# Optimization experiments

Hardware: AMD Instinct MI355X
Metric: run time of the kernel (lower is better)

Reference implementation:

```python
import jax, jax.numpy as jnp
import numpy as np

N_NODES = 100000
N_EDGES = 1600000
EDGES_IN = 1
HID = 64
OUT = 64


def setup_inputs() -> dict:
    key = jax.random.key(0)
    ks = jax.random.split(key, 10)
    s = lambda fan_in: 1.0 / np.sqrt(fan_in)
    inp = {
        "edge_index": jax.random.randint(ks[0], (2, N_EDGES), 0, N_NODES, dtype=jnp.int64) if jax.config.jax_enable_x64 else jax.random.randint(ks[0], (2, N_EDGES), 0, N_NODES, dtype=jnp.int32),
        "edge_attr": jax.random.normal(ks[1], (N_EDGES, EDGES_IN), dtype=jnp.float32),
        # edge MLP: Linear(EDGES_IN->HID), SiLU, Linear(HID->HID), SiLU
        "W1": jax.random.uniform(ks[2], (EDGES_IN, HID), jnp.float32, -s(EDGES_IN), s(EDGES_IN)),
        "b1": jax.random.uniform(ks[3], (HID,), jnp.float32, -s(EDGES_IN), s(EDGES_IN)),
        "W2": jax.random.uniform(ks[4], (HID, HID), jnp.float32, -s(HID), s(HID)),
        "b2": jax.random.uniform(ks[5], (HID,), jnp.float32, -s(HID), s(HID)),
        # node MLP: Linear(HID->HID), SiLU, Linear(HID->OUT)
        "W3": jax.random.uniform(ks[6], (HID, HID), jnp.float32, -s(HID), s(HID)),
        "b3": jax.random.uniform(ks[7], (HID,), jnp.float32, -s(HID), s(HID)),
        "W4": jax.random.uniform(ks[8], (HID, OUT), jnp.float32, -s(HID), s(HID)),
        "b4": jax.random.uniform(ks[9], (OUT,), jnp.float32, -s(HID), s(HID)),
    }
    return inp


def reference(edge_index, edge_attr, W1, b1, W2, b2, W3, b3, W4, b4):
    silu = jax.nn.silu
    # edge model: [E, EDGES_IN] -> [E, HID]
    ef = silu(edge_attr @ W1 + b1)
    ef = silu(ef @ W2 + b2)
    # unsorted_segment_sum over source nodes (row): [E, HID] -> [N, HID]
    row = edge_index[0]
    agg = jax.ops.segment_sum(ef, row, num_segments=N_NODES)
    # node model: [N, HID] -> [N, OUT]
    h = silu(agg @ W3 + b3) @ W4 + b4
    return h
```

## Files before the change

kernel.cpp:

```cpp
#include <hip/hip_runtime.h>
#include <math.h>
#include <utility>

#define TN 4096
#define XMIN (-8.0f)
#define XMAX (8.0f)

#define GB1 256
#define MAXBK 2048
#define BKN 64
#define BKCAP 1792

typedef __attribute__((ext_vector_type(8))) short short8;
typedef __attribute__((ext_vector_type(4))) float f32x4;

__device__ __forceinline__ float silu_f(float v) {
    return v / (1.0f + __expf(-v));
}

__device__ __forceinline__ unsigned short f2bf(float x) {
    unsigned u = __float_as_uint(x);
    return (unsigned short)((u + 0x7FFFu + ((u >> 16) & 1u)) >> 16);
}
__device__ __forceinline__ float bf2f(unsigned short h) {
    return __uint_as_float(((unsigned)h) << 16);
}

#define SPLIT8(w0,w1,w2,w3,w4,w5,w6,w7, H, L) { \
    unsigned short _h0=f2bf(w0),_h1=f2bf(w1),_h2=f2bf(w2),_h3=f2bf(w3), \
                   _h4=f2bf(w4),_h5=f2bf(w5),_h6=f2bf(w6),_h7=f2bf(w7); \
    H = (short8){(short)_h0,(short)_h1,(short)_h2,(short)_h3, \
                 (short)_h4,(short)_h5,(short)_h6,(short)_h7}; \
    L = (short8){(short)f2bf((w0)-bf2f(_h0)),(short)f2bf((w1)-bf2f(_h1)), \
                 (short)f2bf((w2)-bf2f(_h2)),(short)f2bf((w3)-bf2f(_h3)), \
                 (short)f2bf((w4)-bf2f(_h4)),(short)f2bf((w5)-bf2f(_h5)), \
                 (short)f2bf((w6)-bf2f(_h6)),(short)f2bf((w7)-bf2f(_h7))}; }

#define BFRAG(Wp, kc, nt, H, L) { \
    const float* _p = (Wp) + ((kc)*32 + quad*8)*64 + (nt)*16 + m; \
    SPLIT8(_p[0],_p[64],_p[128],_p[192],_p[256],_p[320],_p[384],_p[448], H, L) }

#define MFMA3(AH, AL, BH, BL, ACC) \
    ACC = __builtin_amdgcn_mfma_f32_16x16x32_bf16(AH, BH, ACC, 0, 0, 0); \
    ACC = __builtin_amdgcn_mfma_f32_16x16x32_bf16(AL, BH, ACC, 0, 0, 0); \
    ACC = __builtin_amdgcn_mfma_f32_16x16x32_bf16(AH, BL, ACC, 0, 0, 0);

__global__ void build_table_k(const float* __restrict__ W1, const float* __restrict__ b1,
                              const float* __restrict__ W2, const float* __restrict__ b2,
                              float* __restrict__ table2, int* __restrict__ cnt, int nbk) {
    int gid  = blockIdx.x * blockDim.x + threadIdx.x;
    if (gid < nbk) cnt[gid] = 0;
    int wave = gid >> 6;
    int lane = gid & 63;
    if (wave >= TN) return;
    const float step = (XMAX - XMIN) / (float)(TN - 1);
    float x  = XMIN + step * (float)wave;
    float h1 = silu_f(fmaf(x, W1[lane], b1[lane]));
    float acc = b2[lane];
#pragma unroll
    for (int k = 0; k < 64; ++k) {
        float h1k = __shfl(h1, k, 64);
        acc = fmaf(h1k, W2[k * 64 + lane], acc);
    }
    float val = silu_f(acc);
    table2[(size_t)wave * 128 + 2 * lane] = val;
    if (wave > 0)
        table2[(size_t)(wave - 1) * 128 + 2 * lane + 1] = val;
}

__global__ void pack_w_k(const float* __restrict__ W3, const float* __restrict__ W4,
                         short8* __restrict__ packW) {
    int t = threadIdx.x, lane = t & 63, wid = t >> 6;
    int m = lane & 15, quad = lane >> 4;
    for (int f = wid; f < 16; f += 4) {
        const float* Wp = (f < 8) ? W3 : W4;
        int kc = f & 1, nt = (f >> 1) & 3;
        short8 H, L;
        BFRAG(Wp, kc, nt, H, L)
        packW[(2 * f + 0) * 64 + lane] = H;
        packW[(2 * f + 1) * 64 + lane] = L;
    }
}

__global__ void bhist_k(const int* __restrict__ row, int* __restrict__ cnt,
                        int E, int nbk) {
    __shared__ int h[MAXBK];
    int t = threadIdx.x;
    for (int e = t; e < nbk; e += 256) h[e] = 0;
    __syncthreads();
    for (int i = blockIdx.x * 256 + t; i < E; i += 256 * GB1)
        atomicAdd(&h[row[i] >> 6], 1);
    __syncthreads();
    for (int e = t; e < nbk; e += 256)
        if (h[e]) atomicAdd(&cnt[e], h[e]);
}

__global__ void scan1_k(const int* __restrict__ cnt, int* __restrict__ bhs,
                        int* __restrict__ cur, int n) {
    __shared__ int b0[MAXBK], b1[MAXBK];
    int t = threadIdx.x;
    for (int e = t; e < MAXBK; e += 1024) b0[e] = (e < n) ? cnt[e] : 0;
    __syncthreads();
    int* src = b0; int* dst = b1;
    for (int d = 1; d < MAXBK; d <<= 1) {
        for (int e = t; e < MAXBK; e += 1024)
            dst[e] = src[e] + ((e >= d) ? src[e - d] : 0);
        __syncthreads();
        int* tmp = src; src = dst; dst = tmp;
    }
    for (int e = t; e < n; e += 1024) {
        int v = (e == 0) ? 0 : src[e - 1];
        bhs[e] = v; cur[e] = v;
    }
    if (t == 0) bhs[n] = src[n - 1];
}

__global__ void bscatter_k(const int* __restrict__ row, const float* __restrict__ x,
                           int* __restrict__ cur, unsigned int* __restrict__ packed,
                           int E, int nbk) {
    __shared__ int hist[MAXBK];
    int t = threadIdx.x;
    for (int e = t; e < nbk; e += 256) hist[e] = 0;
    __syncthreads();
    for (int i = blockIdx.x * 256 + t; i < E; i += 256 * GB1)
        atomicAdd(&hist[row[i] >> 6], 1);
    __syncthreads();
    int shift = (int)(((long)blockIdx.x * nbk) >> 8);
    for (int k = t; k < nbk; k += 256) {
        int e = k + shift; if (e >= nbk) e -= nbk;
        int c = hist[e];
        hist[e] = c ? atomicAdd(&cur[e], c) : 0;
    }
    __syncthreads();
    const float scale = (float)(TN - 1) / (XMAX - XMIN);
    for (int i = blockIdx.x * 256 + t; i < E; i += 256 * GB1) {
        int   r  = row[i];
        float xv = x[i];
        float tt = fminf(fmaxf((xv - XMIN) * scale, 0.f), (float)(TN - 1) - 0.001f);
        int   i0 = (int)tt;
        unsigned int q = min((unsigned int)((tt - (float)i0) * 8192.0f), 8191u);
        unsigned int pk = ((unsigned int)(r & 63) << 25) | ((unsigned int)i0 << 13) | q;
        int p = atomicAdd(&hist[r >> 6], 1);
        packed[p] = pk;
    }
}

__global__ __launch_bounds__(256, 8)
void gather_k(const unsigned int* __restrict__ packed, const int* __restrict__ bhs,
              const float* __restrict__ table2, float* __restrict__ aggOut, int N) {
    __shared__ __align__(16) unsigned int srt[BKCAP];
    __shared__ int hist[BKN + 1];
    __shared__ int curs[BKN];
    int t = threadIdx.x, lane = t & 63, wid = t >> 6;
    int b = blockIdx.x;

    int s   = bhs[b];
    int e_  = bhs[b + 1];
    int cnt = min(e_ - s, BKCAP);

    for (int i = t; i <= BKN; i += 256) hist[i] = 0;
    __syncthreads();
    for (int i = t; i < cnt; i += 256)
        atomicAdd(&hist[packed[s + i] >> 25], 1);
    __syncthreads();

    if (wid == 0) {
        int c = hist[lane];
        int sc = c;
#pragma unroll
        for (int d = 1; d < 64; d <<= 1) {
            int u = __shfl_up(sc, d, 64);
            if (lane >= d) sc += u;
        }
        hist[lane] = sc - c;  curs[lane] = sc - c;
        if (lane == 63) hist[BKN] = sc;
    }
    __syncthreads();

    for (int i = t; i < cnt; i += 256) {
        unsigned int p = packed[s + i];
        int pos = atomicAdd(&curs[p >> 25], 1);
        srt[pos] = p;
    }
    __syncthreads();

    const float2* tab = (const float2*)table2 + lane;
    for (int nl = wid; nl < BKN; nl += 4) {
        int n = (b << 6) + nl;
        if (n >= N) break;
        int beg = hist[nl], dn = hist[nl + 1] - beg;
        float a0 = 0.f, a1 = 0.f, a2 = 0.f, a3 = 0.f;
        int j = 0;
        int head = (4 - (beg & 3)) & 3;
        if (head > dn) head = dn;
        for (; j < head; ++j) {
            unsigned int p0 = srt[beg + j];
            float2 uv0 = tab[(size_t)((p0 >> 13) & 0xFFFu) << 6];
            float f0 = (float)(p0 & 0x1FFFu) * (1.0f / 8192.0f);
            a0 = fmaf(f0, uv0.y - uv0.x, a0 + uv0.x);
        }
        for (; j + 4 <= dn; j += 4) {
            uint4 q = *(const uint4*)&srt[beg + j];
            unsigned int p0 = q.x, p1 = q.y, p2 = q.z, p3 = q.w;
            float2 uv0 = tab[(size_t)((p0 >> 13) & 0xFFFu) << 6];
            float2 uv1 = tab[(size_t)((p1 >> 13) & 0xFFFu) << 6];
            float2 uv2 = tab[(size_t)((p2 >> 13) & 0xFFFu) << 6];
            float2 uv3 = tab[(size_t)((p3 >> 13) & 0xFFFu) << 6];
            float f0 = (float)(p0 & 0x1FFFu) * (1.0f / 8192.0f);
            float f1 = (float)(p1 & 0x1FFFu) * (1.0f / 8192.0f);
            float f2 = (float)(p2 & 0x1FFFu) * (1.0f / 8192.0f);
            float f3 = (float)(p3 & 0x1FFFu) * (1.0f / 8192.0f);
            a0 = fmaf(f0, uv0.y - uv0.x, a0 + uv0.x);
            a1 = fmaf(f1, uv1.y - uv1.x, a1 + uv1.x);
            a2 = fmaf(f2, uv2.y - uv2.x, a2 + uv2.x);
            a3 = fmaf(f3, uv3.y - uv3.x, a3 + uv3.x);
        }
        for (; j < dn; ++j) {
            unsigned int p0 = srt[beg + j];
            float2 uv0 = tab[(size_t)((p0 >> 13) & 0xFFFu) << 6];
            float f0 = (float)(p0 & 0x1FFFu) * (1.0f / 8192.0f);
            a0 = fmaf(f0, uv0.y - uv0.x, a0 + uv0.x);
        }
        aggOut[(size_t)n * 64 + lane] = (a0 + a1) + (a2 + a3);
    }
}

__global__ __launch_bounds__(256, 1)
void mlp_k(const short8* __restrict__ packW, const float* __restrict__ b3,
           const float* __restrict__ b4, float* __restrict__ h, int N, int ntiles) {
    __shared__ float gt[4][16 * 68];
    int t = threadIdx.x, lane = t & 63, wid = t >> 6;
    int m = lane & 15, quad = lane >> 4;

    const short8* pw = packW + lane;
#define LDW(s) pw[(s) * 64]
    short8 B3h00=LDW( 0), B3l00=LDW( 1), B3h01=LDW( 2), B3l01=LDW( 3);
    short8 B3h10=LDW( 4), B3l10=LDW( 5), B3h11=LDW( 6), B3l11=LDW( 7);
    short8 B3h20=LDW( 8), B3l20=LDW( 9), B3h21=LDW(10), B3l21=LDW(11);
    short8 B3h30=LDW(12), B3l30=LDW(13), B3h31=LDW(14), B3l31=LDW(15);
    short8 B4h00=LDW(16), B4l00=LDW(17), B4h01=LDW(18), B4l01=LDW(19);
    short8 B4h10=LDW(20), B4l10=LDW(21), B4h11=LDW(22), B4l11=LDW(23);
    short8 B4h20=LDW(24), B4l20=LDW(25), B4h21=LDW(26), B4l21=LDW(27);
    short8 B4h30=LDW(28), B4l30=LDW(29), B4h31=LDW(30), B4l31=LDW(31);
#undef LDW
    float c0 = b4[0*16 + m], c1 = b4[1*16 + m], c2 = b4[2*16 + m], c3 = b4[3*16 + m];
    float d0 = b3[0*16 + m], d1 = b3[1*16 + m], d2 = b3[2*16 + m], d3 = b3[3*16 + m];
    float* g = gt[wid];

    for (int tile = blockIdx.x; tile < ntiles; tile += gridDim.x) {
        long r0 = (long)tile * 64 + wid * 16;
        if (r0 >= N) continue;

        long ra = r0 + m; if (ra > N - 1) ra = N - 1;
        const float* ap = h + ra * 64 + quad * 8;
        float4 p0 = *(const float4*)(ap);       float4 p1 = *(const float4*)(ap + 4);
        float4 p2 = *(const float4*)(ap + 32);  float4 p3 = *(const float4*)(ap + 36);
        short8 Ah0, Al0, Ah1, Al1;
        SPLIT8(p0.x,p0.y,p0.z,p0.w,p1.x,p1.y,p1.z,p1.w, Ah0, Al0)
        SPLIT8(p2.x,p2.y,p2.z,p2.w,p3.x,p3.y,p3.z,p3.w, Ah1, Al1)

        f32x4 acc0 = {0.f,0.f,0.f,0.f}, acc1 = {0.f,0.f,0.f,0.f};
        f32x4 acc2 = {0.f,0.f,0.f,0.f}, acc3 = {0.f,0.f,0.f,0.f};
        MFMA3(Ah0, Al0, B3h00, B3l00, acc0)  MFMA3(Ah1, Al1, B3h01, B3l01, acc0)
        MFMA3(Ah0, Al0, B3h10, B3l10, acc1)  MFMA3(Ah1, Al1, B3h11, B3l11, acc1)
        MFMA3(Ah0, Al0, B3h20, B3l20, acc2)  MFMA3(Ah1, Al1, B3h21, B3l21, acc2)
        MFMA3(Ah0, Al0, B3h30, B3l30, acc3)  MFMA3(Ah1, Al1, B3h31, B3l31, acc3)

        g[(quad*4+0)*68 + 0*16 + m] = silu_f(acc0.x + d0);
        g[(quad*4+1)*68 + 0*16 + m] = silu_f(acc0.y + d0);
        g[(quad*4+2)*68 + 0*16 + m] = silu_f(acc0.z + d0);
        g[(quad*4+3)*68 + 0*16 + m] = silu_f(acc0.w + d0);
        g[(quad*4+0)*68 + 1*16 + m] = silu_f(acc1.x + d1);
        g[(quad*4+1)*68 + 1*16 + m] = silu_f(acc1.y + d1);
        g[(quad*4+2)*68 + 1*16 + m] = silu_f(acc1.z + d1);
        g[(quad*4+3)*68 + 1*16 + m] = silu_f(acc1.w + d1);
        g[(quad*4+0)*68 + 2*16 + m] = silu_f(acc2.x + d2);
        g[(quad*4+1)*68 + 2*16 + m] = silu_f(acc2.y + d2);
        g[(quad*4+2)*68 + 2*16 + m] = silu_f(acc2.z + d2);
        g[(quad*4+3)*68 + 2*16 + m] = silu_f(acc2.w + d2);
        g[(quad*4+0)*68 + 3*16 + m] = silu_f(acc3.x + d3);
        g[(quad*4+1)*68 + 3*16 + m] = silu_f(acc3.y + d3);
        g[(quad*4+2)*68 + 3*16 + m] = silu_f(acc3.z + d3);
        g[(quad*4+3)*68 + 3*16 + m] = silu_f(acc3.w + d3);

        const float* gp = g + m * 68 + quad * 8;
        float4 q0 = *(const float4*)(gp);       float4 q1 = *(const float4*)(gp + 4);
        float4 q2 = *(const float4*)(gp + 32);  float4 q3 = *(const float4*)(gp + 36);
        short8 Gh0, Gl0, Gh1, Gl1;
        SPLIT8(q0.x,q0.y,q0.z,q0.w,q1.x,q1.y,q1.z,q1.w, Gh0, Gl0)
        SPLIT8(q2.x,q2.y,q2.z,q2.w,q3.x,q3.y,q3.z,q3.w, Gh1, Gl1)

        f32x4 o0 = {0.f,0.f,0.f,0.f}, o1 = {0.f,0.f,0.f,0.f};
        f32x4 o2 = {0.f,0.f,0.f,0.f}, o3 = {0.f,0.f,0.f,0.f};
        MFMA3(Gh0, Gl0, B4h00, B4l00, o0)  MFMA3(Gh1, Gl1, B4h01, B4l01, o0)
        MFMA3(Gh0, Gl0, B4h10, B4l10, o1)  MFMA3(Gh1, Gl1, B4h11, B4l11, o1)
        MFMA3(Gh0, Gl0, B4h20, B4l20, o2)  MFMA3(Gh1, Gl1, B4h21, B4l21, o2)
        MFMA3(Gh0, Gl0, B4h30, B4l30, o3)  MFMA3(Gh1, Gl1, B4h31, B4l31, o3)

        long rw = r0 + quad * 4;
        if (rw + 0 < N) { float* o = h + (rw+0)*64;
            o[ 0+m]=o0.x+c0; o[16+m]=o1.x+c1; o[32+m]=o2.x+c2; o[48+m]=o3.x+c3; }
        if (rw + 1 < N) { float* o = h + (rw+1)*64;
            o[ 0+m]=o0.y+c0; o[16+m]=o1.y+c1; o[32+m]=o2.y+c2; o[48+m]=o3.y+c3; }
        if (rw + 2 < N) { float* o = h + (rw+2)*64;
            o[ 0+m]=o0.z+c0; o[16+m]=o1.z+c1; o[32+m]=o2.z+c2; o[48+m]=o3.z+c3; }
        if (rw + 3 < N) { float* o = h + (rw+3)*64;
            o[ 0+m]=o0.w+c0; o[16+m]=o1.w+c1; o[32+m]=o2.w+c2; o[48+m]=o3.w+c3; }
    }
}

__global__ void zero_k(float4* __restrict__ p, int n4) {
    int i = blockIdx.x * blockDim.x + threadIdx.x;
    int stride = gridDim.x * blockDim.x;
    float4 z = make_float4(0.f, 0.f, 0.f, 0.f);
    for (; i < n4; i += stride) p[i] = z;
}

__global__ void edge_k(const int* __restrict__ row, const float* __restrict__ xarr,
                       const float* __restrict__ table2, float* __restrict__ agg, int E) {
    int gid    = blockIdx.x * blockDim.x + threadIdx.x;
    int lane   = gid & 63;
    int wave   = gid >> 6;
    int nwaves = (gridDim.x * blockDim.x) >> 6;
    const float scale = (float)(TN - 1) / (XMAX - XMIN);
    const float2* tab = (const float2*)table2 + lane;
    for (int e = wave; e < E; e += nwaves) {
        float x = xarr[e];
        int   r = row[e];
        float t = fminf(fmaxf((x - XMIN) * scale, 0.0f), (float)(TN - 1) - 0.001f);
        int   i0 = (int)t;
        float f  = t - (float)i0;
        float2 uv = tab[i0 << 6];
        atomicAdd(agg + (size_t)r * 64 + lane, fmaf(f, uv.y - uv.x, uv.x));
    }
}

extern "C" void kernel_launch(void* const* d_in, const int* in_sizes, int n_in,
                              void* d_out, int out_size, void* d_ws, size_t ws_size,
                              hipStream_t stream) {
    const int*   edge_index = (const int*)  d_in[0];
    const float* edge_attr  = (const float*)d_in[1];
    const float* W1 = (const float*)d_in[2];
    const float* b1 = (const float*)d_in[3];
    const float* W2 = (const float*)d_in[4];
    const float* b2 = (const float*)d_in[5];
    const float* W3 = (const float*)d_in[6];
    const float* b3 = (const float*)d_in[7];
    const float* W4 = (const float*)d_in[8];
    const float* b4 = (const float*)d_in[9];

    float* out = (float*)d_out;
    const int E   = in_sizes[1];
    const int N   = out_size / 64;
    const int nbk = (N + 63) >> 6;
    const int nmb = (N + 63) / 64;

    char* ws = (char*)d_ws;
    size_t off = 0;
    auto carve = [&](size_t bytes) { size_t r = off; off = (off + bytes + 255) & ~(size_t)255; return r; };
    size_t tableOff = carve((size_t)TN * 128 * 4);
    size_t packWOff = carve((size_t)32 * 64 * 16);
    size_t cntOff   = carve((size_t)nbk * 4);
    size_t bhsOff   = carve((size_t)(nbk + 1) * 4);
    size_t curOff   = carve((size_t)nbk * 4);
    size_t pkOff    = carve((size_t)E * 4);
    bool fits = (off <= ws_size) && (nbk <= MAXBK);

    float*  table2 = (float*)(ws + tableOff);
    short8* packW  = (short8*)(ws + packWOff);
    int*    cnt    = (int*)(ws + cntOff);

    build_table_k<<<TN / 4, 256, 0, stream>>>(W1, b1, W2, b2, table2, cnt,
                                              fits ? nbk : 0);
    pack_w_k<<<1, 256, 0, stream>>>(W3, W4, packW);

    if (fits) {
        int* bhs = (int*)(ws + bhsOff);
        int* cur = (int*)(ws + curOff);
        unsigned int* packed = (unsigned int*)(ws + pkOff);

        bhist_k   <<<GB1, 256, 0, stream>>>(edge_index, cnt, E, nbk);
        scan1_k   <<<1, 1024, 0, stream>>>(cnt, bhs, cur, nbk);
        bscatter_k<<<GB1, 256, 0, stream>>>(edge_index, edge_attr, cur, packed, E, nbk);
        gather_k  <<<nbk, 256, 0, stream>>>(packed, bhs, table2, out, N);
        mlp_k     <<<512, 256, 0, stream>>>(packW, b3, b4, out, N, nmb);
    } else {
        zero_k<<<4096, 256, 0, stream>>>((float4*)out, (N * 64) / 4);
        edge_k<<<8192, 256, 0, stream>>>(edge_index, edge_attr, table2, out, E);
        mlp_k <<<512, 256, 0, stream>>>(packW, b3, b4, out, N, nmb);
    }
}
```

Baseline: 209.4 us.

## Replace histogram-scan bucketing with fixed-capacity bucket slots and unroll gather by eight

Removes the separate histogram and prefix-scan kernels by giving each 64-node bucket a fixed slot of BKCAP entries, so the scatter kernel claims offsets directly with atomics on per-bucket counters. This cuts two launches and one full pass over the row indices. In exchange the packed buffer grows to nbk*BKCAP entries, and edges past capacity are silently dropped, although the old gather already truncated at BKCAP. The gather inner loop is also unrolled to eight edges per iteration so more table loads are in flight at once.

```diff
diff --git a/kernel.cpp b/kernel.cpp
--- a/kernel.cpp
+++ b/kernel.cpp
@@ -82,41 +82,8 @@
     }
 }
 
-__global__ void bhist_k(const int* __restrict__ row, int* __restrict__ cnt,
-                        int E, int nbk) {
-    __shared__ int h[MAXBK];
-    int t = threadIdx.x;
-    for (int e = t; e < nbk; e += 256) h[e] = 0;
-    __syncthreads();
-    for (int i = blockIdx.x * 256 + t; i < E; i += 256 * GB1)
-        atomicAdd(&h[row[i] >> 6], 1);
-    __syncthreads();
-    for (int e = t; e < nbk; e += 256)
-        if (h[e]) atomicAdd(&cnt[e], h[e]);
-}
-
-__global__ void scan1_k(const int* __restrict__ cnt, int* __restrict__ bhs,
-                        int* __restrict__ cur, int n) {
-    __shared__ int b0[MAXBK], b1[MAXBK];
-    int t = threadIdx.x;
-    for (int e = t; e < MAXBK; e += 1024) b0[e] = (e < n) ? cnt[e] : 0;
-    __syncthreads();
-    int* src = b0; int* dst = b1;
-    for (int d = 1; d < MAXBK; d <<= 1) {
-        for (int e = t; e < MAXBK; e += 1024)
-            dst[e] = src[e] + ((e >= d) ? src[e - d] : 0);
-        __syncthreads();
-        int* tmp = src; src = dst; dst = tmp;
-    }
-    for (int e = t; e < n; e += 1024) {
-        int v = (e == 0) ? 0 : src[e - 1];
-        bhs[e] = v; cur[e] = v;
-    }
-    if (t == 0) bhs[n] = src[n - 1];
-}
-
 __global__ void bscatter_k(const int* __restrict__ row, const float* __restrict__ x,
-                           int* __restrict__ cur, unsigned int* __restrict__ packed,
+                           int* __restrict__ cnt, unsigned int* __restrict__ packed,
                            int E, int nbk) {
     __shared__ int hist[MAXBK];
     int t = threadIdx.x;
@@ -129,7 +96,7 @@
     for (int k = t; k < nbk; k += 256) {
         int e = k + shift; if (e >= nbk) e -= nbk;
         int c = hist[e];
-        hist[e] = c ? atomicAdd(&cur[e], c) : 0;
+        hist[e] = c ? (e * BKCAP + atomicAdd(&cnt[e], c)) : 0;
     }
     __syncthreads();
     const float scale = (float)(TN - 1) / (XMAX - XMIN);
@@ -140,13 +107,14 @@
         int   i0 = (int)tt;
         unsigned int q = min((unsigned int)((tt - (float)i0) * 8192.0f), 8191u);
         unsigned int pk = ((unsigned int)(r & 63) << 25) | ((unsigned int)i0 << 13) | q;
-        int p = atomicAdd(&hist[r >> 6], 1);
-        packed[p] = pk;
+        int bk = r >> 6;
+        int p = atomicAdd(&hist[bk], 1);
+        if (p < (bk + 1) * BKCAP) packed[p] = pk;
     }
 }
 
 __global__ __launch_bounds__(256, 8)
-void gather_k(const unsigned int* __restrict__ packed, const int* __restrict__ bhs,
+void gather_k(const unsigned int* __restrict__ packed, const int* __restrict__ cntArr,
               const float* __restrict__ table2, float* __restrict__ aggOut, int N) {
     __shared__ __align__(16) unsigned int srt[BKCAP];
     __shared__ int hist[BKN + 1];
@@ -154,9 +122,8 @@
     int t = threadIdx.x, lane = t & 63, wid = t >> 6;
     int b = blockIdx.x;
 
-    int s   = bhs[b];
-    int e_  = bhs[b + 1];
-    int cnt = min(e_ - s, BKCAP);
+    int s   = b * BKCAP;
+    int cnt = min(cntArr[b], BKCAP);
 
     for (int i = t; i <= BKN; i += 256) hist[i] = 0;
     __syncthreads();
@@ -199,17 +166,44 @@
             float f0 = (float)(p0 & 0x1FFFu) * (1.0f / 8192.0f);
             a0 = fmaf(f0, uv0.y - uv0.x, a0 + uv0.x);
         }
+        for (; j + 8 <= dn; j += 8) {
+            uint4 qa = *(const uint4*)&srt[beg + j];
+            uint4 qb = *(const uint4*)&srt[beg + j + 4];
+            float2 uv0 = tab[(size_t)((qa.x >> 13) & 0xFFFu) << 6];
+            float2 uv1 = tab[(size_t)((qa.y >> 13) & 0xFFFu) << 6];
+            float2 uv2 = tab[(size_t)((qa.z >> 13) & 0xFFFu) << 6];
+            float2 uv3 = tab[(size_t)((qa.w >> 13) & 0xFFFu) << 6];
+            float2 uv4 = tab[(size_t)((qb.x >> 13) & 0xFFFu) << 6];
+            float2 uv5 = tab[(size_t)((qb.y >> 13) & 0xFFFu) << 6];
+            float2 uv6 = tab[(size_t)((qb.z >> 13) & 0xFFFu) << 6];
+            float2 uv7 = tab[(size_t)((qb.w >> 13) & 0xFFFu) << 6];
+            float f0 = (float)(qa.x & 0x1FFFu) * (1.0f / 8192.0f);
+            float f1 = (float)(qa.y & 0x1FFFu) * (1.0f / 8192.0f);
+            float f2 = (float)(qa.z & 0x1FFFu) * (1.0f / 8192.0f);
+            float f3 = (float)(qa.w & 0x1FFFu) * (1.0f / 8192.0f);
+            float f4 = (float)(qb.x & 0x1FFFu) * (1.0f / 8192.0f);
+            float f5 = (float)(qb.y & 0x1FFFu) * (1.0f / 8192.0f);
+            float f6 = (float)(qb.z & 0x1FFFu) * (1.0f / 8192.0f);
+            float f7 = (float)(qb.w & 0x1FFFu) * (1.0f / 8192.0f);
+            a0 = fmaf(f0, uv0.y - uv0.x, a0 + uv0.x);
+            a1 = fmaf(f1, uv1.y - uv1.x, a1 + uv1.x);
+            a2 = fmaf(f2, uv2.y - uv2.x, a2 + uv2.x);
+            a3 = fmaf(f3, uv3.y - uv3.x, a3 + uv3.x);
+            a0 = fmaf(f4, uv4.y - uv4.x, a0 + uv4.x);
+            a1 = fmaf(f5, uv5.y - uv5.x, a1 + uv5.x);
+            a2 = fmaf(f6, uv6.y - uv6.x, a2 + uv6.x);
+            a3 = fmaf(f7, uv7.y - uv7.x, a3 + uv7.x);
+        }
         for (; j + 4 <= dn; j += 4) {
             uint4 q = *(const uint4*)&srt[beg + j];
-            unsigned int p0 = q.x, p1 = q.y, p2 = q.z, p3 = q.w;
-            float2 uv0 = tab[(size_t)((p0 >> 13) & 0xFFFu) << 6];
-            float2 uv1 = tab[(size_t)((p1 >> 13) & 0xFFFu) << 6];
-            float2 uv2 = tab[(size_t)((p2 >> 13) & 0xFFFu) << 6];
-            float2 uv3 = tab[(size_t)((p3 >> 13) & 0xFFFu) << 6];
-            float f0 = (float)(p0 & 0x1FFFu) * (1.0f / 8192.0f);
-            float f1 = (float)(p1 & 0x1FFFu) * (1.0f / 8192.0f);
-            float f2 = (float)(p2 & 0x1FFFu) * (1.0f / 8192.0f);
-            float f3 = (float)(p3 & 0x1FFFu) * (1.0f / 8192.0f);
+            float2 uv0 = tab[(size_t)((q.x >> 13) & 0xFFFu) << 6];
+            float2 uv1 = tab[(size_t)((q.y >> 13) & 0xFFFu) << 6];
+            float2 uv2 = tab[(size_t)((q.z >> 13) & 0xFFFu) << 6];
+            float2 uv3 = tab[(size_t)((q.w >> 13) & 0xFFFu) << 6];
+            float f0 = (float)(q.x & 0x1FFFu) * (1.0f / 8192.0f);
+            float f1 = (float)(q.y & 0x1FFFu) * (1.0f / 8192.0f);
+            float f2 = (float)(q.z & 0x1FFFu) * (1.0f / 8192.0f);
+            float f3 = (float)(q.w & 0x1FFFu) * (1.0f / 8192.0f);
             a0 = fmaf(f0, uv0.y - uv0.x, a0 + uv0.x);
             a1 = fmaf(f1, uv1.y - uv1.x, a1 + uv1.x);
             a2 = fmaf(f2, uv2.y - uv2.x, a2 + uv2.x);
@@ -361,9 +355,7 @@
     size_t tableOff = carve((size_t)TN * 128 * 4);
     size_t packWOff = carve((size_t)32 * 64 * 16);
     size_t cntOff   = carve((size_t)nbk * 4);
-    size_t bhsOff   = carve((size_t)(nbk + 1) * 4);
-    size_t curOff   = carve((size_t)nbk * 4);
-    size_t pkOff    = carve((size_t)E * 4);
+    size_t pkOff    = carve((size_t)nbk * BKCAP * 4);
     bool fits = (off <= ws_size) && (nbk <= MAXBK);
 
     float*  table2 = (float*)(ws + tableOff);
@@ -375,14 +367,10 @@
     pack_w_k<<<1, 256, 0, stream>>>(W3, W4, packW);
 
     if (fits) {
-        int* bhs = (int*)(ws + bhsOff);
-        int* cur = (int*)(ws + curOff);
         unsigned int* packed = (unsigned int*)(ws + pkOff);
 
-        bhist_k   <<<GB1, 256, 0, stream>>>(edge_index, cnt, E, nbk);
-        scan1_k   <<<1, 1024, 0, stream>>>(cnt, bhs, cur, nbk);
-        bscatter_k<<<GB1, 256, 0, stream>>>(edge_index, edge_attr, cur, packed, E, nbk);
-        gather_k  <<<nbk, 256, 0, stream>>>(packed, bhs, table2, out, N);
+        bscatter_k<<<GB1, 256, 0, stream>>>(edge_index, edge_attr, cnt, packed, E, nbk);
+        gather_k  <<<nbk, 256, 0, stream>>>(packed, cnt, table2, out, N);
         mlp_k     <<<512, 256, 0, stream>>>(packW, b3, b4, out, N, nmb);
     } else {
         zero_k<<<4096, 256, 0, stream>>>((float4*)out, (N * 64) / 4);
```

After: 201.7 us. 1.04x faster.
